# Optimization experiments

Hardware: AMD Instinct MI355X
Metric: run time of the kernel (lower is better)

The kernel has to match this reference:

```python
import jax, jax.numpy as jnp
import numpy as np

N_WIRES = 4
N_LAYERS = 2
B = 16384
EPS = 1e-5


def apply_ry(state, wire, theta):
    # state: (B,2,2,2,2) complex64; theta: scalar or (B,)
    st = jnp.moveaxis(state, wire + 1, 1)
    half = jnp.asarray(theta) * 0.5
    c = jnp.cos(half).reshape(-1, 1, 1, 1).astype(state.dtype)
    s = jnp.sin(half).reshape(-1, 1, 1, 1).astype(state.dtype)
    n0 = c * st[:, 0] - s * st[:, 1]
    n1 = s * st[:, 0] + c * st[:, 1]
    return jnp.moveaxis(jnp.stack([n0, n1], axis=1), 1, wire + 1)


def apply_rz(state, wire, theta):
    st = jnp.moveaxis(state, wire + 1, 1)
    half = jnp.asarray(theta) * 0.5
    c = jnp.cos(half)
    s = jnp.sin(half)
    p0 = (c - 1j * s).reshape(-1, 1, 1, 1).astype(state.dtype)
    p1 = (c + 1j * s).reshape(-1, 1, 1, 1).astype(state.dtype)
    return jnp.moveaxis(jnp.stack([p0 * st[:, 0], p1 * st[:, 1]], axis=1), 1, wire + 1)


def apply_cnot(state, ctrl, tgt):
    st = jnp.moveaxis(state, (ctrl + 1, tgt + 1), (1, 2))
    # flip target where control == 1
    st = jnp.concatenate([st[:, :1], st[:, 1:, ::-1]], axis=1)
    return jnp.moveaxis(st, (1, 2), (ctrl + 1, tgt + 1))


def expect_z(state):
    probs = jnp.real(state * jnp.conj(state))  # (B,2,2,2,2)
    exps = []
    for w in range(N_WIRES):
        p = jnp.moveaxis(probs, w + 1, 1)
        exps.append((p[:, 0] - p[:, 1]).sum(axis=(1, 2, 3)))
    return jnp.stack(exps, axis=-1)  # (B,4)


def quanv(x, qparams):
    bsz = x.shape[0]
    # 2x2 patches in row-major loop order: (B, 196, 4) with [p00,p01,p10,p11]
    patches = x.reshape(bsz, 14, 2, 14, 2).transpose(0, 1, 3, 2, 4).reshape(bsz, 196, 4)
    patches = jnp.transpose(patches, (1, 0, 2))  # (196, B, 4)
    state0 = jnp.zeros((bsz, 2, 2, 2, 2), jnp.complex64).at[:, 0, 0, 0, 0].set(1.0)

    def step(state, vals):
        # NOTE: original code never resets the device between patches -> state carries over
        for i in range(N_WIRES):
            state = apply_ry(state, i, vals[:, i])
        for l in range(N_LAYERS):
            for i in range(N_WIRES):
                state = apply_ry(state, i, qparams[l, i, 0])
                state = apply_rz(state, i, qparams[l, i, 1])
            for i in range(N_WIRES - 1):
                state = apply_cnot(state, i, i + 1)
        return state, expect_z(state)

    _, meas = jax.lax.scan(step, state0, patches)  # (196, B, 4)
    return jnp.transpose(meas, (1, 0, 2)).reshape(bsz, 196 * 4)


def batchnorm(h, g, b):
    # training-mode BatchNorm1d: biased batch statistics
    m = h.mean(axis=0)
    v = h.var(axis=0)
    return g * (h - m) / jnp.sqrt(v + EPS) + b


def setup_inputs() -> dict:
    key = jax.random.key(0)
    ks = jax.random.split(key, 6)
    x = jax.random.uniform(ks[0], (B, 28, 28), dtype=jnp.float32)
    qparams = jax.random.normal(ks[1], (N_LAYERS, N_WIRES, 2), dtype=jnp.float32)
    w1 = jax.random.normal(ks[2], (256, 784), dtype=jnp.float32) * 0.03
    w2 = jax.random.normal(ks[3], (256, 256), dtype=jnp.float32) * 0.05
    w3 = jax.random.normal(ks[4], (10, 256), dtype=jnp.float32) * 0.05
    return {
        "x": x, "qparams": qparams,
        "w1": w1, "b1": jnp.zeros((256,), jnp.float32),
        "g1": jnp.ones((256,), jnp.float32), "be1": jnp.zeros((256,), jnp.float32),
        "w2": w2, "b2": jnp.zeros((256,), jnp.float32),
        "g2": jnp.ones((256,), jnp.float32), "be2": jnp.zeros((256,), jnp.float32),
        "w3": w3, "b3": jnp.zeros((10,), jnp.float32),
    }


def reference(x, qparams, w1, b1, g1, be1, w2, b2, g2, be2, w3, b3):
    feats = quanv(x, qparams)                      # (B, 784)
    h = jax.nn.relu(batchnorm(feats @ w1.T + b1, g1, be1))
    h2 = jax.nn.relu(batchnorm(h @ w2.T + b2, g2, be2)) + h
    return jax.nn.log_softmax(h2 @ w3.T + b3, axis=-1)
```

## Files before the change

kernel.cpp:

```cpp
#include <hip/hip_runtime.h>
#include <math.h>

#define BQ 16384
#define KFP 800
#define NH 256
#define NCLS 10

typedef float f32x4 __attribute__((ext_vector_type(4)));
typedef unsigned int u32x2 __attribute__((ext_vector_type(2)));
typedef unsigned int u32x4 __attribute__((ext_vector_type(4)));
typedef __bf16 bf16x8 __attribute__((ext_vector_type(8)));
typedef __bf16 bf16x4 __attribute__((ext_vector_type(4)));


template<int ST>
__device__ __forceinline__ void u_ry(float* sr, float* si, float c, float s) {
#pragma unroll
  for (int i = 0; i < 16; i++) {
    if (i & ST) continue;
    const int j = i | ST;
    const float a0r = sr[i], a0i = si[i], a1r = sr[j], a1i = si[j];
    sr[i] = c * a0r - s * a1r;  si[i] = c * a0i - s * a1i;
    sr[j] = s * a0r + c * a1r;  si[j] = s * a0i + c * a1i;
  }
}
template<int ST>
__device__ __forceinline__ void u_rz(float* sr, float* si, float c, float s) {
#pragma unroll
  for (int i = 0; i < 16; i++) {
    const float pz = (i & ST) ? s : -s;
    const float ar = sr[i], ai = si[i];
    sr[i] = c * ar - pz * ai;
    si[i] = c * ai + pz * ar;
  }
}
template<int SC, int STG>
__device__ __forceinline__ void u_cnot(float* sr, float* si) {
#pragma unroll
  for (int i = 0; i < 16; i++) {
    if (!(i & SC) || (i & STG)) continue;
    const int j = i | STG;
    float t;
    t = sr[i]; sr[i] = sr[j]; sr[j] = t;
    t = si[i]; si[i] = si[j]; si[j] = t;
  }
}

__global__ __launch_bounds__(256) void prep_kernel(
    const float* __restrict__ qp, const float* __restrict__ w1,
    const float* __restrict__ w2, __bf16* __restrict__ Abuf,
    __bf16* __restrict__ w1b, __bf16* __restrict__ w2b,
    float* __restrict__ gs1, float* __restrict__ gs2) {
  const int bid = blockIdx.x;
  const int tid = threadIdx.x;
  if (bid == 0) {
    gs1[tid] = 0.f; gs1[256 + tid] = 0.f;
    gs2[tid] = 0.f; gs2[256 + tid] = 0.f;
    __shared__ float Ur[16][16], Ui[16][16];
    if (tid < 16) {
      float sr[16], si[16];
#pragma unroll
      for (int i = 0; i < 16; i++) { sr[i] = (i == tid) ? 1.f : 0.f; si[i] = 0.f; }
#pragma unroll
      for (int l = 0; l < 2; l++) {
        { const float t = qp[l*8 + 0] * 0.5f; u_ry<8>(sr, si, cosf(t), sinf(t)); }
        { const float t = qp[l*8 + 1] * 0.5f; u_rz<8>(sr, si, cosf(t), sinf(t)); }
        { const float t = qp[l*8 + 2] * 0.5f; u_ry<4>(sr, si, cosf(t), sinf(t)); }
        { const float t = qp[l*8 + 3] * 0.5f; u_rz<4>(sr, si, cosf(t), sinf(t)); }
        { const float t = qp[l*8 + 4] * 0.5f; u_ry<2>(sr, si, cosf(t), sinf(t)); }
        { const float t = qp[l*8 + 5] * 0.5f; u_rz<2>(sr, si, cosf(t), sinf(t)); }
        { const float t = qp[l*8 + 6] * 0.5f; u_ry<1>(sr, si, cosf(t), sinf(t)); }
        { const float t = qp[l*8 + 7] * 0.5f; u_rz<1>(sr, si, cosf(t), sinf(t)); }
        u_cnot<8, 4>(sr, si);
        u_cnot<4, 2>(sr, si);
        u_cnot<2, 1>(sr, si);
      }
#pragma unroll
      for (int r = 0; r < 16; r++) { Ur[r][tid] = sr[r]; Ui[r][tid] = si[r]; }
    }
    __syncthreads();
    for (int f = tid; f < 2048; f += 256) {
      const int m   = f & 7;
      const int row = (f >> 3) & 15;
      const int kg  = (f >> 7) & 3;
      const int hl  = (f >> 9) & 1;
      const int t   = (f >> 10) & 1;
      const int k   = kg * 8 + m;
      const int ri_o  = (row >> 2) & 1;
      const int amp_o = ((row >> 3) & 1) * 8 + t * 4 + (row & 3);
      const int ri_i  = (k >> 3) & 1;
      const int amp_i = ((k >> 4) & 1) * 8 + (m >> 2) * 4 + (m & 3);
      const float u_r = Ur[amp_o][amp_i], u_i = Ui[amp_o][amp_i];
      float v = (ri_o == 0) ? ((ri_i == 0) ? u_r : -u_i)
                            : ((ri_i == 0) ? u_i : u_r);
      if (hl) {
        const __bf16 hb = (__bf16)v;
        v = v - (float)hb;
      }
      Abuf[f] = (__bf16)v;
    }
  } else if (bid <= 256) {
    const int r = bid - 1;
    for (int c = tid; c < KFP; c += 256)
      w1b[r * KFP + c] = (c < 784) ? (__bf16)w1[r * 784 + c] : (__bf16)0.f;
  } else {
    const int base = (bid - 257) * 2048 + tid * 8;
    const float4 v0 = *(const float4*)(w2 + base);
    const float4 v1 = *(const float4*)(w2 + base + 4);
    bf16x8 o = {(__bf16)v0.x, (__bf16)v0.y, (__bf16)v0.z, (__bf16)v0.w,
                (__bf16)v1.x, (__bf16)v1.y, (__bf16)v1.z, (__bf16)v1.w};
    *(bf16x8*)(w2b + base) = o;
  }
}


__device__ __forceinline__ float swz16(float v) {
  return __int_as_float(__builtin_amdgcn_ds_swizzle(__float_as_int(v), 0x401F));
}
__device__ __forceinline__ float plsum(float v) {
  const u32x2 r = __builtin_amdgcn_permlane32_swap(
      __float_as_uint(v), __float_as_uint(v), false, false);
  return __uint_as_float(r.x) + __uint_as_float(r.y);
}
__device__ __forceinline__ float plpick(float v, bool r0sel) {
  const u32x2 r = __builtin_amdgcn_permlane32_swap(
      __float_as_uint(v), __float_as_uint(v), false, false);
  return __uint_as_float(r0sel ? r.x : r.y);
}

__global__ __launch_bounds__(256) void quanv_mfma(
    const float* __restrict__ x, const __bf16* __restrict__ Abuf,
    __bf16* __restrict__ feats) {
  const int tid = threadIdx.x;
  const int l = tid & 63;
  const int wv = tid >> 6;
  const int col = l & 15;
  const int kg = l >> 4;
  const int b = blockIdx.x * 64 + wv * 16 + col;
  const float* xb = x + (size_t)b * 784;
  __bf16* fb = feats + (size_t)b * KFP;
  const float sg0 = (l & 32) ? 1.f : -1.f;

  const u32x2 pt = __builtin_amdgcn_permlane32_swap((unsigned)l, (unsigned)l,
                                                    false, false);
  const bool p32r0 = (pt.x == (unsigned)(l ^ 32));

  const bf16x8* Ab = (const bf16x8*)Abuf;
  const bf16x8 A0h = Ab[(0 * 4 + kg) * 16 + col];
  const bf16x8 A0l = Ab[(1 * 4 + kg) * 16 + col];
  const bf16x8 A1h = Ab[(2 * 4 + kg) * 16 + col];
  const bf16x8 A1l = Ab[(3 * 4 + kg) * 16 + col];

  f32x4 c0 = {(kg == 0) ? 1.f : 0.f, 0.f, 0.f, 0.f};
  f32x4 c1 = {0.f, 0.f, 0.f, 0.f};
  const f32x4 z4 = {0.f, 0.f, 0.f, 0.f};

  float ts0, tw1, tw2, tw3, gsc;
  auto trig = [&](float2 a, float2 b2) {
    const float h0 = a.x * 0.5f, h1 = a.y * 0.5f;
    const float h2 = b2.x * 0.5f, h3 = b2.y * 0.5f;
    const float c0_ = __cosf(h0), s0_ = __sinf(h0);
    const float c1_ = __cosf(h1), s1_ = __sinf(h1);
    const float c2_ = __cosf(h2), s2_ = __sinf(h2);
    const float c3_ = __cosf(h3), s3_ = __sinf(h3);
    ts0 = sg0 * __fdividef(s0_, c0_);
    tw1 = __fdividef(s1_, c1_);
    tw2 = __fdividef(s2_, c2_);
    tw3 = __fdividef(s3_, c3_);
    gsc = (c0_ * c1_) * (c2_ * c3_);
  };

  auto meas = [&](__bf16* dst) {
    const float sq0 = c0.x * c0.x, sq1 = c0.y * c0.y;
    const float sq2 = c0.z * c0.z, sq3 = c0.w * c0.w;
    const float sq4 = c1.x * c1.x, sq5 = c1.y * c1.y;
    const float sq6 = c1.z * c1.z, sq7 = c1.w * c1.w;
    const float s01 = sq0 + sq1, s23 = sq2 + sq3;
    const float s45 = sq4 + sq5, s67 = sq6 + sq7;
    const float d01 = sq0 - sq1, d23 = sq2 - sq3;
    const float d45 = sq4 - sq5, d67 = sq6 - sq7;
    const float z3 = (d01 + d23) + (d45 + d67);
    const float z2 = (s01 - s23) + (s45 - s67);
    const float q03 = s01 + s23, q47 = s45 + s67;
    const float z1 = q03 - q47;
    const float T  = q03 + q47;
    const float z3a = z3 + swz16(z3);
    const float z2a = z2 + swz16(z2);
    const float z1a = z1 + swz16(z1);
    const float Ta  = -sg0 * (T + swz16(T));
    const float z3f = plsum(z3a);
    const float z2f = plsum(z2a);
    const float z1f = plsum(z1a);
    const float z0f = plsum(Ta);
    if (kg == 0) {
      bf16x4 o = {(__bf16)z0f, (__bf16)z1f, (__bf16)z2f, (__bf16)z3f};
      *(bf16x4*)dst = o;
    }
  };

  auto step = [&]() {
    float S[8] = {c0.x, c0.y, c0.z, c0.w, c1.x, c1.y, c1.z, c1.w};
#pragma unroll
    for (int j = 0; j < 4; j++) {
      const float a = S[j];
      S[j]     = fmaf(-tw1, S[4 + j], S[j]);
      S[4 + j] = fmaf( tw1, a,        S[4 + j]);
    }
#pragma unroll
    for (int base = 0; base < 8; base += 4)
#pragma unroll
      for (int j = 0; j < 2; j++) {
        const int i0 = base + j, i1 = base + j + 2;
        const float a = S[i0];
        S[i0] = fmaf(-tw2, S[i1], S[i0]);
        S[i1] = fmaf( tw2, a,     S[i1]);
      }
#pragma unroll
    for (int i0 = 0; i0 < 8; i0 += 2) {
      const float a = S[i0];
      S[i0]     = fmaf(-tw3, S[i0 + 1], S[i0]);
      S[i0 + 1] = fmaf( tw3, a,         S[i0 + 1]);
    }
#pragma unroll
    for (int i = 0; i < 8; i++) {
      const float P = plpick(S[i], p32r0);
      S[i] = fmaf(ts0, P, S[i]);
    }
    unsigned gb[8], lb[8];
#pragma unroll
    for (int i = 0; i < 8; i++) {
      const float GS = gsc * S[i];
      const unsigned bb = __float_as_uint(GS);
      gb[i] = bb;
      lb[i] = __float_as_uint(GS - __uint_as_float(bb & 0xFFFF0000u));
    }
    u32x4 bhv, blv;
#pragma unroll
    for (int j = 0; j < 4; j++) {
      bhv[j] = __builtin_amdgcn_perm(gb[2 * j + 1], gb[2 * j], 0x07060302u);
      blv[j] = __builtin_amdgcn_perm(lb[2 * j + 1], lb[2 * j], 0x07060302u);
    }
    const bf16x8 Bh = __builtin_bit_cast(bf16x8, bhv);
    const bf16x8 Bl = __builtin_bit_cast(bf16x8, blv);
    f32x4 p0 = __builtin_amdgcn_mfma_f32_16x16x32_bf16(A0h, Bh, z4, 0, 0, 0);
    f32x4 q0 = __builtin_amdgcn_mfma_f32_16x16x32_bf16(A0l, Bh, z4, 0, 0, 0);
    q0 = __builtin_amdgcn_mfma_f32_16x16x32_bf16(A0h, Bl, q0, 0, 0, 0);
    f32x4 p1 = __builtin_amdgcn_mfma_f32_16x16x32_bf16(A1h, Bh, z4, 0, 0, 0);
    f32x4 q1 = __builtin_amdgcn_mfma_f32_16x16x32_bf16(A1l, Bh, z4, 0, 0, 0);
    q1 = __builtin_amdgcn_mfma_f32_16x16x32_bf16(A1h, Bl, q1, 0, 0, 0);
    c0 = p0 + q0;
    c1 = p1 + q1;
  };

  float2 t0 = *(const float2*)(xb);
  float2 t1 = *(const float2*)(xb + 28);
  trig(t0, t1);
  t0 = *(const float2*)(xb + 2);
  t1 = *(const float2*)(xb + 30);
  step();
  trig(t0, t1);
  t0 = *(const float2*)(xb + 4);
  t1 = *(const float2*)(xb + 32);
  int nrr = 0, ncc = 3;
  __bf16* fp = fb;

#pragma unroll 2
  for (int it = 1; it < 196; ++it) {
    const float* np = (it < 194) ? (xb + 56 * nrr + 2 * ncc) : xb;
    const float2 n0 = *(const float2*)np;
    const float2 n1 = *(const float2*)(np + 28);
    ncc++;
    if (ncc == 14) { ncc = 0; nrr++; }

    meas(fp); fp += 4;
    step();
    trig(t0, t1);
    t0 = n0; t1 = n1;
  }
  meas(fp);

  if (kg == 0) {
    *(uint4*)(fb + 784) = (uint4){0, 0, 0, 0};
    *(uint4*)(fb + 792) = (uint4){0, 0, 0, 0};
  }
}

#define GBM 128
#define GBN 64
#define GBK 32

__device__ __forceinline__ void gld16(const void* g, void* l) {
  __builtin_amdgcn_global_load_lds(
      (const __attribute__((address_space(1))) unsigned int*)g,
      (__attribute__((address_space(3))) unsigned int*)l, 16, 0, 0);
}

__global__ __launch_bounds__(256) void gemm_bf16_nt(
    const __bf16* __restrict__ A, const __bf16* __restrict__ B,
    const float* __restrict__ bias, __bf16* __restrict__ C,
    int M, int N, int K, float* __restrict__ gstats) {
  __shared__ char lds[24576];
  const int tid = threadIdx.x;
  const int nwg = gridDim.x;
  const int sid = (blockIdx.x & 7) * (nwg >> 3) + (blockIdx.x >> 3);
  const int bm = (sid >> 2) * GBM;
  const int bn = (sid & 3) * GBN;
  const int NK = K / GBK;
  const size_t lda = (size_t)K * 2;

  const int srow = tid >> 2;
  const int lc16 = tid & 3;
  const int ag0 = lc16 ^ ((srow >> 1) & 3);
  const int ag1 = lc16 ^ (((srow + 64) >> 1) & 3);
  const char* a0p = (const char*)A + (size_t)(bm + srow) * lda + ag0 * 16;
  const char* a1p = (const char*)A + (size_t)(bm + 64 + srow) * lda + ag1 * 16;
  const char* b0p = (const char*)B + (size_t)(bn + srow) * lda + ag0 * 16;

  const int wid = tid >> 6, lane = tid & 63;
  const int wr = wid >> 1, wc = wid & 1;
  const int ln15 = lane & 15, ln4 = lane >> 4;
  int aoff[4], boff[2];
#pragma unroll
  for (int m = 0; m < 4; m++) {
    const int row = wr * 64 + m * 16 + ln15;
    aoff[m] = row * 64 + ((ln4 ^ ((row >> 1) & 3)) * 16);
  }
#pragma unroll
  for (int n = 0; n < 2; n++) {
    const int row = wc * 32 + n * 16 + ln15;
    boff[n] = 16384 + row * 64 + ((ln4 ^ ((row >> 1) & 3)) * 16);
  }

  f32x4 acc[4][2];
#pragma unroll
  for (int m = 0; m < 4; m++)
#pragma unroll
    for (int n = 0; n < 2; n++) acc[m][n] = (f32x4){0.f, 0.f, 0.f, 0.f};

  auto stage = [&](int buf, int kt) {
    const size_t kb = (size_t)kt * GBK * 2;
    char* as = lds + buf * 8192 + tid * 16;
    char* bs = lds + 16384 + buf * 4096 + tid * 16;
    gld16(a0p + kb, as);
    gld16(a1p + kb, as + 4096);
    gld16(b0p + kb, bs);
  };

  stage(0, 0);
  for (int kt = 0; kt < NK; kt++) {
    __syncthreads();
    if (kt + 1 < NK) stage((kt + 1) & 1, kt + 1);
    const int ab = (kt & 1) * 8192, bb = (kt & 1) * 4096;
    bf16x8 af[4], bfr[2];
#pragma unroll
    for (int m = 0; m < 4; m++) af[m] = *(const bf16x8*)(lds + ab + aoff[m]);
#pragma unroll
    for (int n = 0; n < 2; n++) bfr[n] = *(const bf16x8*)(lds + bb + boff[n]);
#pragma unroll
    for (int m = 0; m < 4; m++)
#pragma unroll
      for (int n = 0; n < 2; n++)
        acc[m][n] = __builtin_amdgcn_mfma_f32_16x16x32_bf16(af[m], bfr[n], acc[m][n], 0, 0, 0);
  }

  float csum[2], csq[2];
#pragma unroll
  for (int n = 0; n < 2; n++) {
    const int ccol = bn + wc * 32 + n * 16 + ln15;
    const float bv = bias[ccol];
    float s = 0.f, ss = 0.f;
#pragma unroll
    for (int m = 0; m < 4; m++) {
      const int crow = bm + wr * 64 + m * 16 + ln4 * 4;
#pragma unroll
      for (int r = 0; r < 4; r++) {
        const float v = acc[m][n][r] + bv;
        C[(size_t)(crow + r) * N + ccol] = (__bf16)v;
        s += v; ss += v * v;
      }
    }
    csum[n] = s; csq[n] = ss;
  }
  __syncthreads();
  float* sred = (float*)lds;
#pragma unroll
  for (int n = 0; n < 2; n++) {
    const int slot = wid * 128 + ln4 * 32 + n * 16 + ln15;
    sred[slot] = csum[n];
    sred[512 + slot] = csq[n];
  }
  __syncthreads();
  if (tid < 128) {
    const int colb = tid & 63, which = tid >> 6;
    const int wcc = colb >> 5, c31 = colb & 31;
    float a = 0.f;
    const int base = which * 512 + c31;
#pragma unroll
    for (int w2_ = 0; w2_ < 2; w2_++)
#pragma unroll
      for (int l4 = 0; l4 < 4; l4++)
        a += sred[base + (w2_ * 2 + wcc) * 128 + l4 * 32];
    atomicAdd(&gstats[(bn + colb) * 2 + which], a);
  }
}

__global__ __launch_bounds__(256) void bn1_relu(
    const __bf16* __restrict__ h1p, __bf16* __restrict__ h1b,
    const float* __restrict__ gstats, const float* __restrict__ g,
    const float* __restrict__ be) {
  __shared__ float as[NH], cs[NH];
  {
    const int t = threadIdx.x;
    const float s = gstats[t * 2], ss = gstats[t * 2 + 1];
    const float mean = s * (1.f / 16384.f);
    const float var = ss * (1.f / 16384.f) - mean * mean;
    const float a = g[t] * rsqrtf(var + 1e-5f);
    as[t] = a;
    cs[t] = be[t] - mean * a;
  }
  __syncthreads();
  const size_t i = (size_t)blockIdx.x * 256 + threadIdx.x;
  const bf16x8 v = *(const bf16x8*)(h1p + i * 8);
  const int colb = (int)((i * 8) & (NH - 1));
  bf16x8 o;
#pragma unroll
  for (int j = 0; j < 8; j++)
    o[j] = (__bf16)fmaxf(fmaf((float)v[j], as[colb + j], cs[colb + j]), 0.f);
  *(bf16x8*)(h1b + i * 8) = o;
}

__global__ __launch_bounds__(256) void tail_fused(
    const __bf16* __restrict__ h2b, const __bf16* __restrict__ h1b,
    const float* __restrict__ gstats, const float* __restrict__ g,
    const float* __restrict__ be, const float* __restrict__ w3,
    const float* __restrict__ b3, float* __restrict__ out) {
  __shared__ float w3s[NCLS * NH];
  __shared__ float as[NH], cs[NH];
  for (int i = threadIdx.x; i < NCLS * NH; i += 256) w3s[i] = w3[i];
  {
    const int t = threadIdx.x;
    const float s = gstats[t * 2], ss = gstats[t * 2 + 1];
    const float mean = s * (1.f / 16384.f);
    const float var = ss * (1.f / 16384.f) - mean * mean;
    const float a = g[t] * rsqrtf(var + 1e-5f);
    as[t] = a;
    cs[t] = be[t] - mean * a;
  }
  __syncthreads();

  const int m = blockIdx.x * 256 + threadIdx.x;
  const __bf16* hr = h2b + (size_t)m * NH;
  const __bf16* rr = h1b + (size_t)m * NH;
  float acc[NCLS];
#pragma unroll
  for (int n = 0; n < NCLS; n++) acc[n] = b3[n];

  for (int k = 0; k < NH; k += 8) {
    const bf16x8 hv = *(const bf16x8*)(hr + k);
    const bf16x8 rv = *(const bf16x8*)(rr + k);
    float v[8];
#pragma unroll
    for (int j = 0; j < 8; j++)
      v[j] = fmaxf(fmaf((float)hv[j], as[k + j], cs[k + j]), 0.f) + (float)rv[j];
#pragma unroll
    for (int n = 0; n < NCLS; n++) {
      float d = 0.f;
#pragma unroll
      for (int j = 0; j < 8; j++) d = fmaf(v[j], w3s[n * NH + k + j], d);
      acc[n] += d;
    }
  }

  float mx = acc[0];
#pragma unroll
  for (int n = 1; n < NCLS; n++) mx = fmaxf(mx, acc[n]);
  float se = 0.f;
#pragma unroll
  for (int n = 0; n < NCLS; n++) se += expf(acc[n] - mx);
  const float lse = logf(se) + mx;
#pragma unroll
  for (int n = 0; n < NCLS; n++) out[(size_t)m * NCLS + n] = acc[n] - lse;
}

extern "C" void kernel_launch(void* const* d_in, const int* in_sizes, int n_in,
                              void* d_out, int out_size, void* d_ws, size_t ws_size,
                              hipStream_t stream) {
  const float* x   = (const float*)d_in[0];
  const float* qp  = (const float*)d_in[1];
  const float* w1  = (const float*)d_in[2];
  const float* b1  = (const float*)d_in[3];
  const float* g1  = (const float*)d_in[4];
  const float* be1 = (const float*)d_in[5];
  const float* w2  = (const float*)d_in[6];
  const float* b2  = (const float*)d_in[7];
  const float* g2  = (const float*)d_in[8];
  const float* be2 = (const float*)d_in[9];
  const float* w3  = (const float*)d_in[10];
  const float* b3  = (const float*)d_in[11];
  float* out = (float*)d_out;

  char* w = (char*)d_ws;
  __bf16* feats = (__bf16*)w;
  __bf16* h1p   = (__bf16*)(w + 26214400);
  __bf16* h1b   = (__bf16*)(w + 34603008);
  __bf16* h2b   = (__bf16*)(w + 42991616);
  __bf16* w1b   = (__bf16*)(w + 51380224);
  __bf16* w2b   = (__bf16*)(w + 51789824);
  float*  gs1   = (float*)(w + 51920896);
  float*  gs2   = (float*)(w + 51922944);
  __bf16* Abuf  = (__bf16*)(w + 51924992);

  prep_kernel<<<289, 256, 0, stream>>>(qp, w1, w2, Abuf, w1b, w2b, gs1, gs2);
  quanv_mfma<<<BQ / 64, 256, 0, stream>>>(x, Abuf, feats);

  gemm_bf16_nt<<<(BQ / GBM) * (NH / GBN), 256, 0, stream>>>(
      feats, w1b, b1, h1p, BQ, NH, KFP, gs1);
  bn1_relu<<<(BQ * NH / 8) / 256, 256, 0, stream>>>(h1p, h1b, gs1, g1, be1);

  gemm_bf16_nt<<<(BQ / GBM) * (NH / GBN), 256, 0, stream>>>(
      h1b, w2b, b2, h2b, BQ, NH, NH, gs2);

  tail_fused<<<BQ / 256, 256, 0, stream>>>(h2b, h1b, gs2, g2, be2, w3, b3, out);
}
```

Before: 205.9 us.

## Fuse first GEMM and BN statistics into quanvolution kernel, drop feats buffer

The quanvolution kernel now packs its measured features directly into MFMA A-fragments in registers. Every 8 patches it issues 16 MFMAs against W1 fragments loaded from global memory, so it computes the first linear layer in-kernel. It adds the bias, reduces batchnorm sum and sum-of-squares through LDS with atomics, and writes h1p via an LDS-staged tile. This removes the 26 MB feature round trip and a separate GEMM launch. In exchange it uses many more registers (64 accumulators plus 16 B fragments, launch bounds 256,1), which lowers occupancy, and it keeps one block per 64 rows that reloads W1 from global memory each time.

```diff
diff --git a/kernel.cpp b/kernel.cpp
--- a/kernel.cpp
+++ b/kernel.cpp
@@ -127,10 +127,15 @@
       __float_as_uint(v), __float_as_uint(v), false, false);
   return __uint_as_float(r0sel ? r.x : r.y);
 }
-
-__global__ __launch_bounds__(256) void quanv_mfma(
+__device__ __forceinline__ unsigned bfbits(float v) {
+  return (unsigned)__builtin_bit_cast(unsigned short, (__bf16)v);
+}
+
+__global__ __launch_bounds__(256, 1) void quanv_fused(
     const float* __restrict__ x, const __bf16* __restrict__ Abuf,
-    __bf16* __restrict__ feats) {
+    const __bf16* __restrict__ w1b, const float* __restrict__ b1,
+    __bf16* __restrict__ h1p, float* __restrict__ gs1) {
+  __shared__ char qlds[33792];
   const int tid = threadIdx.x;
   const int l = tid & 63;
   const int wv = tid >> 6;
@@ -138,7 +143,6 @@
   const int kg = l >> 4;
   const int b = blockIdx.x * 64 + wv * 16 + col;
   const float* xb = x + (size_t)b * 784;
-  __bf16* fb = feats + (size_t)b * KFP;
   const float sg0 = (l & 32) ? 1.f : -1.f;
 
   const u32x2 pt = __builtin_amdgcn_permlane32_swap((unsigned)l, (unsigned)l,
@@ -154,6 +158,26 @@
   f32x4 c0 = {(kg == 0) ? 1.f : 0.f, 0.f, 0.f, 0.f};
   f32x4 c1 = {0.f, 0.f, 0.f, 0.f};
   const f32x4 z4 = {0.f, 0.f, 0.f, 0.f};
+
+  u32x4 frag = {0, 0, 0, 0};
+  bf16x8 bfrag[16];
+  f32x4 acc[16];
+#pragma unroll
+  for (int nt = 0; nt < 16; nt++) acc[nt] = z4;
+
+  auto loadB = [&](int w8) {
+#pragma unroll
+    for (int nt = 0; nt < 16; nt++)
+      bfrag[nt] = *(const bf16x8*)(w1b + (size_t)(nt * 16 + col) * KFP +
+                                   w8 * 32 + kg * 8);
+  };
+  auto burst = [&]() {
+    const bf16x8 fa = __builtin_bit_cast(bf16x8, frag);
+#pragma unroll
+    for (int nt = 0; nt < 16; nt++)
+      acc[nt] = __builtin_amdgcn_mfma_f32_16x16x32_bf16(fa, bfrag[nt], acc[nt], 0, 0, 0);
+    frag = (u32x4){0, 0, 0, 0};
+  };
 
   float ts0, tw1, tw2, tw3, gsc;
   auto trig = [&](float2 a, float2 b2) {
@@ -170,7 +194,7 @@
     gsc = (c0_ * c1_) * (c2_ * c3_);
   };
 
-  auto meas = [&](__bf16* dst) {
+  auto meas = [&](int mit) {
     const float sq0 = c0.x * c0.x, sq1 = c0.y * c0.y;
     const float sq2 = c0.z * c0.z, sq3 = c0.w * c0.w;
     const float sq4 = c1.x * c1.x, sq5 = c1.y * c1.y;
@@ -192,10 +216,15 @@
     const float z2f = plsum(z2a);
     const float z1f = plsum(z1a);
     const float z0f = plsum(Ta);
-    if (kg == 0) {
-      bf16x4 o = {(__bf16)z0f, (__bf16)z1f, (__bf16)z2f, (__bf16)z3f};
-      *(bf16x4*)dst = o;
-    }
+    const unsigned zlo = (bfbits(z1f) << 16) | bfbits(z0f);
+    const unsigned zhi = (bfbits(z3f) << 16) | bfbits(z2f);
+    const int p = mit & 7;
+    const bool selA = ((p >> 1) == kg) & ((p & 1) == 0);
+    const bool selB = ((p >> 1) == kg) & ((p & 1) == 1);
+    frag.x = selA ? zlo : frag.x;
+    frag.y = selA ? zhi : frag.y;
+    frag.z = selB ? zlo : frag.z;
+    frag.w = selB ? zhi : frag.w;
   };
 
   auto step = [&]() {
@@ -226,22 +255,14 @@
       const float P = plpick(S[i], p32r0);
       S[i] = fmaf(ts0, P, S[i]);
     }
-    unsigned gb[8], lb[8];
+    bf16x8 Bh, Bl;
 #pragma unroll
     for (int i = 0; i < 8; i++) {
       const float GS = gsc * S[i];
-      const unsigned bb = __float_as_uint(GS);
-      gb[i] = bb;
-      lb[i] = __float_as_uint(GS - __uint_as_float(bb & 0xFFFF0000u));
-    }
-    u32x4 bhv, blv;
-#pragma unroll
-    for (int j = 0; j < 4; j++) {
-      bhv[j] = __builtin_amdgcn_perm(gb[2 * j + 1], gb[2 * j], 0x07060302u);
-      blv[j] = __builtin_amdgcn_perm(lb[2 * j + 1], lb[2 * j], 0x07060302u);
-    }
-    const bf16x8 Bh = __builtin_bit_cast(bf16x8, bhv);
-    const bf16x8 Bl = __builtin_bit_cast(bf16x8, blv);
+      const __bf16 hb = (__bf16)GS;
+      Bh[i] = hb;
+      Bl[i] = (__bf16)(GS - (float)hb);
+    }
     f32x4 p0 = __builtin_amdgcn_mfma_f32_16x16x32_bf16(A0h, Bh, z4, 0, 0, 0);
     f32x4 q0 = __builtin_amdgcn_mfma_f32_16x16x32_bf16(A0l, Bh, z4, 0, 0, 0);
     q0 = __builtin_amdgcn_mfma_f32_16x16x32_bf16(A0h, Bl, q0, 0, 0, 0);
@@ -252,6 +273,7 @@
     c1 = p1 + q1;
   };
 
+  loadB(0);
   float2 t0 = *(const float2*)(xb);
   float2 t1 = *(const float2*)(xb + 28);
   trig(t0, t1);
@@ -262,9 +284,7 @@
   t0 = *(const float2*)(xb + 4);
   t1 = *(const float2*)(xb + 32);
   int nrr = 0, ncc = 3;
-  __bf16* fp = fb;
-
-#pragma unroll 2
+
   for (int it = 1; it < 196; ++it) {
     const float* np = (it < 194) ? (xb + 56 * nrr + 2 * ncc) : xb;
     const float2 n0 = *(const float2*)np;
@@ -272,16 +292,60 @@
     ncc++;
     if (ncc == 14) { ncc = 0; nrr++; }
 
-    meas(fp); fp += 4;
+    meas(it - 1);
+    if ((it & 7) == 0) {
+      burst();
+      loadB(it >> 3);
+    }
     step();
     trig(t0, t1);
     t0 = n0; t1 = n1;
   }
-  meas(fp);
-
-  if (kg == 0) {
-    *(uint4*)(fb + 784) = (uint4){0, 0, 0, 0};
-    *(uint4*)(fb + 792) = (uint4){0, 0, 0, 0};
+  meas(195);
+  burst();
+
+  float bv[16];
+#pragma unroll
+  for (int nt = 0; nt < 16; nt++) bv[nt] = b1[nt * 16 + col];
+  float* sredS = (float*)qlds;
+  float* sredQ = sredS + 4096;
+#pragma unroll
+  for (int nt = 0; nt < 16; nt++) {
+    float s = 0.f, q = 0.f;
+#pragma unroll
+    for (int r = 0; r < 4; r++) {
+      const float v = acc[nt][r] + bv[nt];
+      s += v; q += v * v;
+    }
+    sredS[(wv * 4 + kg) * 256 + nt * 16 + col] = s;
+    sredQ[(wv * 4 + kg) * 256 + nt * 16 + col] = q;
+  }
+  __syncthreads();
+  {
+    float s = 0.f, q = 0.f;
+#pragma unroll
+    for (int r = 0; r < 16; r++) {
+      s += sredS[r * 256 + tid];
+      q += sredQ[r * 256 + tid];
+    }
+    atomicAdd(&gs1[tid * 2], s);
+    atomicAdd(&gs1[tid * 2 + 1], q);
+  }
+  __syncthreads();
+
+  __bf16* tile = (__bf16*)qlds;
+#pragma unroll
+  for (int nt = 0; nt < 16; nt++)
+#pragma unroll
+    for (int r = 0; r < 4; r++)
+      tile[(wv * 16 + kg * 4 + r) * 264 + nt * 16 + col] =
+          (__bf16)(acc[nt][r] + bv[nt]);
+  __syncthreads();
+  for (int pass = 0; pass < 8; pass++) {
+    const int idx = pass * 256 + tid;
+    const int row = idx >> 5, c8 = idx & 31;
+    const bf16x8 vv = *(const bf16x8*)&tile[row * 264 + c8 * 8];
+    *(bf16x8*)(h1p + ((size_t)(blockIdx.x * 64 + row)) * 256 + c8 * 8) = vv;
   }
 }
 
@@ -500,21 +564,19 @@
   float* out = (float*)d_out;
 
   char* w = (char*)d_ws;
-  __bf16* feats = (__bf16*)w;
-  __bf16* h1p   = (__bf16*)(w + 26214400);
-  __bf16* h1b   = (__bf16*)(w + 34603008);
-  __bf16* h2b   = (__bf16*)(w + 42991616);
-  __bf16* w1b   = (__bf16*)(w + 51380224);
-  __bf16* w2b   = (__bf16*)(w + 51789824);
-  float*  gs1   = (float*)(w + 51920896);
-  float*  gs2   = (float*)(w + 51922944);
-  __bf16* Abuf  = (__bf16*)(w + 51924992);
+  __bf16* h1p   = (__bf16*)w;
+  __bf16* h1b   = (__bf16*)(w + 8388608);
+  __bf16* h2b   = (__bf16*)(w + 16777216);
+  __bf16* w1b   = (__bf16*)(w + 25165824);
+  __bf16* w2b   = (__bf16*)(w + 25575424);
+  float*  gs1   = (float*)(w + 25706496);
+  float*  gs2   = (float*)(w + 25708544);
+  __bf16* Abuf  = (__bf16*)(w + 25710592);
 
   prep_kernel<<<289, 256, 0, stream>>>(qp, w1, w2, Abuf, w1b, w2b, gs1, gs2);
-  quanv_mfma<<<BQ / 64, 256, 0, stream>>>(x, Abuf, feats);
-
-  gemm_bf16_nt<<<(BQ / GBM) * (NH / GBN), 256, 0, stream>>>(
-      feats, w1b, b1, h1p, BQ, NH, KFP, gs1);
+
+  quanv_fused<<<BQ / 64, 256, 0, stream>>>(x, Abuf, w1b, b1, h1p, gs1);
+
   bn1_relu<<<(BQ * NH / 8) / 256, 256, 0, stream>>>(h1p, h1b, gs1, g1, be1);
 
   gemm_bf16_nt<<<(BQ / GBM) * (NH / GBN), 256, 0, stream>>>(
```

Result: faster. 194.5 us (median of 2 runs) (-5.5%).
